# Performance work log

Hardware: AMD Instinct MI355X
Metric: run time of the kernel (lower is better)

## Reference

```python
import jax, jax.numpy as jnp
import numpy as np

NEG_SLOPE = 0.2


def _add_self_loops(src, dst, n_nodes):
    loop = jnp.arange(n_nodes, dtype=src.dtype)
    return jnp.concatenate([src, loop]), jnp.concatenate([dst, loop])


def _gat_conv(x, W, a_src, a_dst, b, src, dst, n_nodes):
    # Linear transform: [N, F_out]
    h = x @ W
    # Per-node attention halves (heads=1)
    alpha_src = h @ a_src  # [N]
    alpha_dst = h @ a_dst  # [N]
    # Per-edge logits (gather) + LeakyReLU
    e = jax.nn.leaky_relu(alpha_src[src] + alpha_dst[dst], NEG_SLOPE)  # [E]
    # Segment softmax over incoming edges of each destination node
    m = jax.ops.segment_max(e, dst, num_segments=n_nodes)
    e = jnp.exp(e - m[dst])
    s = jax.ops.segment_sum(e, dst, num_segments=n_nodes)
    alpha = e / (s[dst] + 1e-16)  # [E]
    # Weighted scatter-add aggregation
    out = jax.ops.segment_sum(h[src] * alpha[:, None], dst, num_segments=n_nodes)
    return out + b


def setup_inputs() -> dict:
    key = jax.random.key(0)
    ks = jax.random.split(key, 10)
    N, E, D_IN, D_HID, D_OUT = 100000, 3200000, 128, 128, 64
    x = jax.random.normal(ks[0], (N, D_IN), dtype=jnp.float32)
    edge_index = jax.random.randint(ks[1], (2, E), 0, N, dtype=jnp.int64)
    # Glorot-ish scaled params
    W1 = jax.random.normal(ks[2], (D_IN, D_HID), dtype=jnp.float32) / np.sqrt(D_IN)
    a1_src = jax.random.normal(ks[3], (D_HID,), dtype=jnp.float32) / np.sqrt(D_HID)
    a1_dst = jax.random.normal(ks[4], (D_HID,), dtype=jnp.float32) / np.sqrt(D_HID)
    b1 = jnp.zeros((D_HID,), dtype=jnp.float32)
    W2 = jax.random.normal(ks[5], (D_HID, D_OUT), dtype=jnp.float32) / np.sqrt(D_HID)
    a2_src = jax.random.normal(ks[6], (D_OUT,), dtype=jnp.float32) / np.sqrt(D_OUT)
    a2_dst = jax.random.normal(ks[7], (D_OUT,), dtype=jnp.float32) / np.sqrt(D_OUT)
    b2 = jnp.zeros((D_OUT,), dtype=jnp.float32)
    return {"x": x, "edge_index": edge_index, "W1": W1, "a1_src": a1_src,
            "a1_dst": a1_dst, "b1": b1, "W2": W2, "a2_src": a2_src,
            "a2_dst": a2_dst, "b2": b2}


def reference(x, edge_index, W1, a1_src, a1_dst, b1, W2, a2_src, a2_dst, b2):
    n_nodes = x.shape[0]
    # PyG GATConv default: add self-loops
    src, dst = _add_self_loops(edge_index[0], edge_index[1], n_nodes)
    h = jax.nn.relu(_gat_conv(x, W1, a1_src, a1_dst, b1, src, dst, n_nodes))
    h = _gat_conv(h, W2, a2_src, a2_dst, b2, src, dst, n_nodes)
    return jnp.mean(h, axis=0)  # [output_dim]
```

## Files before the change

### kernel.cpp

```cpp
#include <hip/hip_runtime.h>
#include <cstdint>
#include <cstddef>

#define LEAKY_SLOPE 0.2f

typedef __attribute__((ext_vector_type(8))) short short8;
typedef __attribute__((ext_vector_type(4))) float f32x4;

static __device__ inline unsigned short f2b(float f) {
  union { float f; unsigned int u; } c; c.f = f;
  unsigned int u = c.u;
  unsigned int r = (u + 0x7fffu + ((u >> 16) & 1u)) >> 16;
  return (unsigned short)r;
}
static __device__ inline float b2f(unsigned short b) {
  union { unsigned int u; float f; } c; c.u = ((unsigned int)b) << 16;
  return c.f;
}
static __device__ inline unsigned char f2f8(float v) {
  int pk = __builtin_amdgcn_cvt_pk_fp8_f32(v, v, 0, false);
  return (unsigned char)(pk & 0xff);
}
static __device__ inline void fma8f8(float* acc, uint2 u, float w) {
  auto a = __builtin_amdgcn_cvt_pk_f32_fp8(u.x, false);
  auto b = __builtin_amdgcn_cvt_pk_f32_fp8(u.x, true);
  auto c = __builtin_amdgcn_cvt_pk_f32_fp8(u.y, false);
  auto d = __builtin_amdgcn_cvt_pk_f32_fp8(u.y, true);
  acc[0] += w * a[0]; acc[1] += w * a[1];
  acc[2] += w * b[0]; acc[3] += w * b[1];
  acc[4] += w * c[0]; acc[5] += w * c[1];
  acc[6] += w * d[0]; acc[7] += w * d[1];
}

__global__ __launch_bounds__(256) void k_bhist(const int* __restrict__ dst,
                                               int* __restrict__ gcount,
                                               int E, int N, int NB) {
  __shared__ int lh[512];
  for (int i = threadIdx.x; i < NB; i += 256) lh[i] = 0;
  __syncthreads();
  int stride = gridDim.x * blockDim.x;
  for (int idx = blockIdx.x * blockDim.x + threadIdx.x; idx < E + N; idx += stride) {
    int d = (idx < E) ? dst[idx] : (idx - E);
    atomicAdd(&lh[d >> 8], 1);
  }
  __syncthreads();
  for (int i = threadIdx.x; i < NB; i += 256)
    if (lh[i]) atomicAdd(&gcount[i], lh[i]);
}

__global__ __launch_bounds__(512) void k_bscan(const int* __restrict__ gcount,
                                               int* __restrict__ gbase,
                                               int* __restrict__ gcursor,
                                               int NB, int ET, int* __restrict__ offN) {
  __shared__ int sm[512];
  int t = threadIdx.x;
  int v = (t < NB) ? gcount[t] : 0;
  sm[t] = v;
  __syncthreads();
  for (int o = 1; o < 512; o <<= 1) {
    int x = (t >= o) ? sm[t - o] : 0;
    __syncthreads();
    sm[t] += x;
    __syncthreads();
  }
  if (t < NB) {
    int b = sm[t] - v;
    gbase[t] = b;
    gcursor[t] = b;
  }
  if (t == 0) { gbase[NB] = ET; *offN = ET; }
}

template <int CHUNK>
__global__ __launch_bounds__(256) void k_binpass(const int* __restrict__ src,
                                                 const int* __restrict__ dst,
                                                 int* __restrict__ gcursor,
                                                 unsigned int* __restrict__ staging,
                                                 int E, int N, int NB) {
  __shared__ int lh[512];
  __shared__ int lbase[512];
  const int t = threadIdx.x;
  const int ET = E + N;
  const int e0 = blockIdx.x * CHUNK;
  const int e1 = min(e0 + CHUNK, ET);
  for (int i = t; i < NB; i += 256) lh[i] = 0;
  __syncthreads();
  for (int i = e0 + t; i < e1; i += 256) {
    int d = (i < E) ? dst[i] : (i - E);
    atomicAdd(&lh[d >> 8], 1);
  }
  __syncthreads();
  for (int i = t; i < NB; i += 256) {
    int c = lh[i];
    lbase[i] = c ? atomicAdd(&gcursor[i], c) : 0;
    lh[i] = 0;
  }
  __syncthreads();
  for (int i = e0 + t; i < e1; i += 256) {
    int s, d;
    if (i < E) { s = src[i]; d = dst[i]; }
    else       { s = d = i - E; }
    int b = d >> 8;
    int r = atomicAdd(&lh[b], 1);
    staging[lbase[b] + r] = ((unsigned int)s << 8) | (unsigned int)(d & 255);
  }
}

__global__ __launch_bounds__(256) void k_csrbuild(const int* __restrict__ gbase,
                                                  const unsigned int* __restrict__ staging,
                                                  int* __restrict__ off,
                                                  int* __restrict__ csr,
                                                  int N) {
  __shared__ int sc[256];
  __shared__ int cur[256];
  const int b = blockIdx.x, t = threadIdx.x;
  const int s0 = gbase[b], s1 = gbase[b + 1];
  cur[t] = 0;
  __syncthreads();
  for (int i = s0 + t; i < s1; i += 256)
    atomicAdd(&cur[staging[i] & 255], 1);
  __syncthreads();
  int v = cur[t];
  sc[t] = v;
  __syncthreads();
  for (int o = 1; o < 256; o <<= 1) {
    int x = (t >= o) ? sc[t - o] : 0;
    __syncthreads();
    sc[t] += x;
    __syncthreads();
  }
  int excl = s0 + sc[t] - v;
  int node = b * 256 + t;
  if (node < N) off[node] = excl;
  __syncthreads();
  cur[t] = excl;
  __syncthreads();
  for (int i = s0 + t; i < s1; i += 256) {
    unsigned int pv = staging[i];
    int slot = atomicAdd(&cur[pv & 255], 1);
    csr[slot] = (int)(pv >> 8);
  }
}

__global__ __launch_bounds__(256) void k_prep_w(const float* __restrict__ W1,
                                                const float* __restrict__ W2,
                                                unsigned short* __restrict__ W1t,
                                                unsigned short* __restrict__ W2t) {
  int t = threadIdx.x;
  for (int o = t; o < 128 * 128; o += 256) {
    int n = o >> 7, k = o & 127;
    W1t[o] = f2b(W1[k * 128 + n]);
  }
  for (int o = t; o < 64 * 128; o += 256) {
    int n = o >> 7, k = o & 127;
    W2t[o] = f2b(W2[k * 64 + n]);
  }
}

template <int COLS, bool SRC_F32>
__global__ __launch_bounds__(256) void k_gemm_bf16(const void* __restrict__ Ap,
                                                   const unsigned short* __restrict__ Bt,
                                                   unsigned char* __restrict__ C,
                                                   const float* __restrict__ av_src,
                                                   const float* __restrict__ av_dst,
                                                   float* __restrict__ as_,
                                                   float* __restrict__ ad_,
                                                   int N) {
  constexpr int K = 128;
  constexpr int LDA = K + 8;
  __shared__ __align__(16) unsigned short As[64 * LDA];
  __shared__ __align__(16) unsigned short Bs[COLS * LDA];
  const int t = threadIdx.x;
  const int wave = t >> 6, lane = t & 63;
  const int row0 = blockIdx.x * 64;

#pragma unroll
  for (int i = 0; i < 4; ++i) {
    int c = t + 256 * i;
    int r = c >> 4, cq = c & 15;
    int4 v = make_int4(0, 0, 0, 0);
    if (row0 + r < N) {
      if constexpr (SRC_F32) {
        const float* Ar = (const float*)Ap + (size_t)(row0 + r) * K + cq * 8;
        float4 u = *reinterpret_cast<const float4*>(Ar);
        float4 w = *reinterpret_cast<const float4*>(Ar + 4);
        v.x = (int)f2b(u.x) | ((int)f2b(u.y) << 16);
        v.y = (int)f2b(u.z) | ((int)f2b(u.w) << 16);
        v.z = (int)f2b(w.x) | ((int)f2b(w.y) << 16);
        v.w = (int)f2b(w.z) | ((int)f2b(w.w) << 16);
      } else {
        v = *reinterpret_cast<const int4*>((const unsigned short*)Ap +
                                           (size_t)(row0 + r) * K + cq * 8);
      }
    }
    *reinterpret_cast<int4*>(&As[r * LDA + cq * 8]) = v;
  }
#pragma unroll
  for (int i = 0; i < COLS / 16; ++i) {
    int c = t + 256 * i;
    int r = c >> 4, cq = c & 15;
    *reinterpret_cast<int4*>(&Bs[r * LDA + cq * 8]) =
        *reinterpret_cast<const int4*>(Bt + (size_t)r * K + cq * 8);
  }
  __syncthreads();

  const int m15 = lane & 15;
  const int koff = (lane >> 4) * 8;
  const int arow = wave * 16 + m15;

  f32x4 acc[COLS / 16];
#pragma unroll
  for (int ct = 0; ct < COLS / 16; ++ct) acc[ct] = (f32x4){0.f, 0.f, 0.f, 0.f};

#pragma unroll
  for (int kk = 0; kk < K / 32; ++kk) {
    short8 af = *reinterpret_cast<const short8*>(&As[arow * LDA + kk * 32 + koff]);
#pragma unroll
    for (int ct = 0; ct < COLS / 16; ++ct) {
      short8 bf = *reinterpret_cast<const short8*>(&Bs[(ct * 16 + m15) * LDA + kk * 32 + koff]);
      acc[ct] = __builtin_amdgcn_mfma_f32_16x16x32_bf16(af, bf, acc[ct], 0, 0, 0);
    }
  }

#pragma unroll
  for (int ct = 0; ct < COLS / 16; ++ct) {
#pragma unroll
    for (int r = 0; r < 4; ++r) {
      int grow = row0 + wave * 16 + (lane >> 4) * 4 + r;
      if (grow < N)
        C[(size_t)grow * COLS + ct * 16 + m15] = f2f8(acc[ct][r]);
    }
  }

  {
    float ps[4] = {0.f, 0.f, 0.f, 0.f}, pd[4] = {0.f, 0.f, 0.f, 0.f};
#pragma unroll
    for (int ct = 0; ct < COLS / 16; ++ct) {
      float av = av_src[ct * 16 + m15];
      float bv = av_dst[ct * 16 + m15];
#pragma unroll
      for (int r = 0; r < 4; ++r) {
        ps[r] += acc[ct][r] * av;
        pd[r] += acc[ct][r] * bv;
      }
    }
#pragma unroll
    for (int o = 1; o < 16; o <<= 1) {
#pragma unroll
      for (int r = 0; r < 4; ++r) {
        ps[r] += __shfl_xor(ps[r], o);
        pd[r] += __shfl_xor(pd[r], o);
      }
    }
    if (m15 == 0) {
#pragma unroll
      for (int r = 0; r < 4; ++r) {
        int grow = row0 + wave * 16 + (lane >> 4) * 4 + r;
        if (grow < N) { as_[grow] = ps[r]; ad_[grow] = pd[r]; }
      }
    }
  }
}

template <int F, int DEPTH, bool RELU, bool OUT_BF16>
__global__ __launch_bounds__(256) void k_agg(const int* __restrict__ off,
                                             const int* __restrict__ csr,
                                             const float* __restrict__ as_,
                                             const float* __restrict__ ad_,
                                             const unsigned char* __restrict__ h,
                                             const float* __restrict__ bias,
                                             void* __restrict__ outp, int N) {
  constexpr int LPR = F / 8;
  constexpr int GPI = 64 / LPR;
  int wid = (blockIdx.x * blockDim.x + threadIdx.x) >> 6;
  int lane = threadIdx.x & 63;
  if (wid >= N) return;
  const int s0 = off[wid], s1 = off[wid + 1];
  const float adv = ad_[wid];
  const int g  = lane / LPR;
  const int fl = lane % LPR;
  const unsigned char* hb = h + (size_t)fl * 8;

  float acc[8] = {0.f, 0.f, 0.f, 0.f, 0.f, 0.f, 0.f, 0.f};
  float lsum = 0.f;

  for (int base = s0; base < s1; base += 64) {
    int i = base + lane;
    int sv = 0;
    float wexp = 0.f;
    if (i < s1) {
      sv = csr[i];
      float e = as_[sv] + adv;
      e = (e > 0.f) ? e : LEAKY_SLOPE * e;
      wexp = __expf(e);
      lsum += wexp;
    }
    const int jn = min(64, s1 - base);
    int jj = 0;
    for (; jj + DEPTH * GPI <= jn; jj += DEPTH * GPI) {
      int sj[DEPTH];
      float wv[DEPTH];
      uint2 u[DEPTH];
#pragma unroll
      for (int k = 0; k < DEPTH; ++k) {
        sj[k] = __shfl(sv, jj + g + k * GPI);
        wv[k] = __shfl(wexp, jj + g + k * GPI);
      }
#pragma unroll
      for (int k = 0; k < DEPTH; ++k)
        u[k] = *reinterpret_cast<const uint2*>(hb + (size_t)sj[k] * F);
#pragma unroll
      for (int k = 0; k < DEPTH; ++k)
        fma8f8(acc, u[k], wv[k]);
    }
    for (; jj < jn; jj += GPI) {
      int sj0 = __shfl(sv, jj + g);
      float w0 = __shfl(wexp, jj + g);
      uint2 u0 = *reinterpret_cast<const uint2*>(hb + (size_t)sj0 * F);
      fma8f8(acc, u0, w0);
    }
  }

  for (int o = 32; o; o >>= 1) lsum += __shfl_xor(lsum, o);
  const float inv_s = 1.f / (lsum + 1e-16f);

#pragma unroll
  for (int o = LPR; o < 64; o <<= 1) {
#pragma unroll
    for (int k = 0; k < 8; ++k) acc[k] += __shfl_xor(acc[k], o);
  }

  if (g == 0) {
    float ov[8];
#pragma unroll
    for (int k = 0; k < 8; ++k) {
      ov[k] = acc[k] * inv_s + bias[fl * 8 + k];
      if (RELU) ov[k] = fmaxf(ov[k], 0.f);
    }
    if constexpr (OUT_BF16) {
      int4 pk;
      pk.x = (int)f2b(ov[0]) | ((int)f2b(ov[1]) << 16);
      pk.y = (int)f2b(ov[2]) | ((int)f2b(ov[3]) << 16);
      pk.z = (int)f2b(ov[4]) | ((int)f2b(ov[5]) << 16);
      pk.w = (int)f2b(ov[6]) | ((int)f2b(ov[7]) << 16);
      *reinterpret_cast<int4*>((unsigned short*)outp + (size_t)wid * F + fl * 8) = pk;
    } else {
      float* op = (float*)outp + (size_t)wid * F + fl * 8;
      *reinterpret_cast<float4*>(op) = make_float4(ov[0], ov[1], ov[2], ov[3]);
      *reinterpret_cast<float4*>(op + 4) = make_float4(ov[4], ov[5], ov[6], ov[7]);
    }
  }
}

__global__ __launch_bounds__(256) void k_mean(const float* __restrict__ out2,
                                              float* __restrict__ d_out, int N) {
  int c = threadIdx.x & 63;
  int w = threadIdx.x >> 6;
  float acc = 0.f;
  for (int r = blockIdx.x * 4 + w; r < N; r += gridDim.x * 4)
    acc += out2[(size_t)r * 64 + c];
  atomicAdd(&d_out[c], acc * (1.0f / (float)N));
}

extern "C" void kernel_launch(void* const* d_in, const int* in_sizes, int n_in,
                              void* d_out, int out_size, void* d_ws, size_t ws_size,
                              hipStream_t stream) {
  (void)n_in; (void)out_size; (void)ws_size;
  const float* x      = (const float*)d_in[0];
  const int*   edges  = (const int*)d_in[1];
  const float* W1     = (const float*)d_in[2];
  const float* a1_src = (const float*)d_in[3];
  const float* a1_dst = (const float*)d_in[4];
  const float* b1     = (const float*)d_in[5];
  const float* W2     = (const float*)d_in[6];
  const float* a2_src = (const float*)d_in[7];
  const float* a2_dst = (const float*)d_in[8];
  const float* b2     = (const float*)d_in[9];
  float* out = (float*)d_out;

  const int N = in_sizes[0] / 128;
  const int E = in_sizes[1] / 2;
  const int ET = E + N;
  const int NB = (N + 255) >> 8;

  const int* e_src = edges;
  const int* e_dst = edges + E;

  char* ws = (char*)d_ws;
  size_t o = 0;
  auto alloc = [&](size_t bytes) {
    size_t p = o;
    o += (bytes + 511) & ~(size_t)511;
    return p;
  };
  unsigned char*  h1f = (unsigned char*)(ws + alloc((size_t)N * 128));
  unsigned short* g1b = (unsigned short*)(ws + alloc((size_t)N * 128 * 2));
  unsigned char*  h2f = (unsigned char*)(ws + alloc((size_t)N * 64));
  float* out2   = (float*)(ws + alloc((size_t)N * 64 * 4));
  float* as1    = (float*)(ws + alloc((size_t)N * 4));
  float* ad1    = (float*)(ws + alloc((size_t)N * 4));
  float* as2    = (float*)(ws + alloc((size_t)N * 4));
  float* ad2    = (float*)(ws + alloc((size_t)N * 4));
  int*   off    = (int*)(ws + alloc((size_t)(N + 1) * 4));
  int*   gcount = (int*)(ws + alloc((size_t)(NB + 1) * 4));
  int*   gbase  = (int*)(ws + alloc((size_t)(NB + 1) * 4));
  int*   gcursor= (int*)(ws + alloc((size_t)(NB + 1) * 4));
  unsigned int* staging = (unsigned int*)(ws + alloc((size_t)ET * 4));
  int*   csr    = (int*)(ws + alloc((size_t)ET * 4));
  unsigned short* W1t = (unsigned short*)(ws + alloc((size_t)128 * 128 * 2));
  unsigned short* W2t = (unsigned short*)(ws + alloc((size_t)64 * 128 * 2));

  hipMemsetAsync(gcount, 0, (size_t)NB * 4, stream);
  k_bhist<<<512, 256, 0, stream>>>(e_dst, gcount, E, N, NB);
  k_bscan<<<1, 512, 0, stream>>>(gcount, gbase, gcursor, NB, ET, off + N);
  constexpr int CHUNK = 8192;
  k_binpass<CHUNK><<<(ET + CHUNK - 1) / CHUNK, 256, 0, stream>>>(
      e_src, e_dst, gcursor, staging, E, N, NB);
  k_csrbuild<<<NB, 256, 0, stream>>>(gbase, staging, off, csr, N);

  k_prep_w<<<1, 256, 0, stream>>>(W1, W2, W1t, W2t);

  const int gemm_grid = (N + 63) / 64;
  const int node_wave_grid = (N + 3) / 4;

  k_gemm_bf16<128, true><<<gemm_grid, 256, 0, stream>>>(
      x, W1t, h1f, a1_src, a1_dst, as1, ad1, N);
  k_agg<128, 8, true, true><<<node_wave_grid, 256, 0, stream>>>(
      off, csr, as1, ad1, h1f, b1, (void*)g1b, N);

  k_gemm_bf16<64, false><<<gemm_grid, 256, 0, stream>>>(
      g1b, W2t, h2f, a2_src, a2_dst, as2, ad2, N);
  k_agg<64, 4, false, false><<<node_wave_grid, 256, 0, stream>>>(
      off, csr, as2, ad2, h2f, b2, (void*)out2, N);

  hipMemsetAsync(out, 0, 64 * sizeof(float), stream);
  k_mean<<<256, 256, 0, stream>>>(out2, out, N);
}
```

Measured before the change: 445.3 us.

## Collapse second GAT layer into per-source coefficients using linearity of mean

The second layer's full aggregation and GEMM are replaced by an algebraic shortcut. Because the output is a mean over nodes, it equals W2 applied to a coefficient-weighted sum of layer-1 features plus b2, where each coefficient is the sum of the normalized attention weights on a source's out-edges. Layer-2 attention logits are computed in the layer-1 aggregation epilogue through the precomputed vectors W2·a2_src and W2·a2_dst, and a coefficient kernel scatters them with atomics. This removes the 64-wide edge gather and the N×64 intermediate, at the cost of scattered float atomics and small numeric differences in accumulation order. The layer-1 accumulation is also rewritten to use packed two-wide float FMAs.

```diff
diff --git a/kernel.cpp b/kernel.cpp
--- a/kernel.cpp
+++ b/kernel.cpp
@@ -6,6 +6,7 @@
 
 typedef __attribute__((ext_vector_type(8))) short short8;
 typedef __attribute__((ext_vector_type(4))) float f32x4;
+typedef __attribute__((ext_vector_type(2))) float f32x2;
 
 static __device__ inline unsigned short f2b(float f) {
   union { float f; unsigned int u; } c; c.f = f;
@@ -20,16 +21,6 @@
 static __device__ inline unsigned char f2f8(float v) {
   int pk = __builtin_amdgcn_cvt_pk_fp8_f32(v, v, 0, false);
   return (unsigned char)(pk & 0xff);
-}
-static __device__ inline void fma8f8(float* acc, uint2 u, float w) {
-  auto a = __builtin_amdgcn_cvt_pk_f32_fp8(u.x, false);
-  auto b = __builtin_amdgcn_cvt_pk_f32_fp8(u.x, true);
-  auto c = __builtin_amdgcn_cvt_pk_f32_fp8(u.y, false);
-  auto d = __builtin_amdgcn_cvt_pk_f32_fp8(u.y, true);
-  acc[0] += w * a[0]; acc[1] += w * a[1];
-  acc[2] += w * b[0]; acc[3] += w * b[1];
-  acc[4] += w * c[0]; acc[5] += w * c[1];
-  acc[6] += w * d[0]; acc[7] += w * d[1];
 }
 
 __global__ __launch_bounds__(256) void k_bhist(const int* __restrict__ dst,
@@ -144,29 +135,37 @@
 
 __global__ __launch_bounds__(256) void k_prep_w(const float* __restrict__ W1,
                                                 const float* __restrict__ W2,
+                                                const float* __restrict__ a2_src,
+                                                const float* __restrict__ a2_dst,
                                                 unsigned short* __restrict__ W1t,
-                                                unsigned short* __restrict__ W2t) {
+                                                float* __restrict__ va_s,
+                                                float* __restrict__ va_d) {
   int t = threadIdx.x;
   for (int o = t; o < 128 * 128; o += 256) {
     int n = o >> 7, k = o & 127;
     W1t[o] = f2b(W1[k * 128 + n]);
   }
-  for (int o = t; o < 64 * 128; o += 256) {
-    int n = o >> 7, k = o & 127;
-    W2t[o] = f2b(W2[k * 64 + n]);
-  }
-}
-
-template <int COLS, bool SRC_F32>
-__global__ __launch_bounds__(256) void k_gemm_bf16(const void* __restrict__ Ap,
-                                                   const unsigned short* __restrict__ Bt,
-                                                   unsigned char* __restrict__ C,
-                                                   const float* __restrict__ av_src,
-                                                   const float* __restrict__ av_dst,
-                                                   float* __restrict__ as_,
-                                                   float* __restrict__ ad_,
-                                                   int N) {
-  constexpr int K = 128;
+  if (t < 128) {
+    float s = 0.f, d = 0.f;
+    for (int c = 0; c < 64; ++c) {
+      float w = W2[t * 64 + c];
+      s += w * a2_src[c];
+      d += w * a2_dst[c];
+    }
+    va_s[t] = s;
+    va_d[t] = d;
+  }
+}
+
+__global__ __launch_bounds__(256) void k_gemm1(const float* __restrict__ Ap,
+                                               const unsigned short* __restrict__ Bt,
+                                               unsigned char* __restrict__ C,
+                                               const float* __restrict__ av_src,
+                                               const float* __restrict__ av_dst,
+                                               float* __restrict__ as_,
+                                               float* __restrict__ ad_,
+                                               int N) {
+  constexpr int K = 128, COLS = 128;
   constexpr int LDA = K + 8;
   __shared__ __align__(16) unsigned short As[64 * LDA];
   __shared__ __align__(16) unsigned short Bs[COLS * LDA];
@@ -180,18 +179,13 @@
     int r = c >> 4, cq = c & 15;
     int4 v = make_int4(0, 0, 0, 0);
     if (row0 + r < N) {
-      if constexpr (SRC_F32) {
-        const float* Ar = (const float*)Ap + (size_t)(row0 + r) * K + cq * 8;
-        float4 u = *reinterpret_cast<const float4*>(Ar);
-        float4 w = *reinterpret_cast<const float4*>(Ar + 4);
-        v.x = (int)f2b(u.x) | ((int)f2b(u.y) << 16);
-        v.y = (int)f2b(u.z) | ((int)f2b(u.w) << 16);
-        v.z = (int)f2b(w.x) | ((int)f2b(w.y) << 16);
-        v.w = (int)f2b(w.z) | ((int)f2b(w.w) << 16);
-      } else {
-        v = *reinterpret_cast<const int4*>((const unsigned short*)Ap +
-                                           (size_t)(row0 + r) * K + cq * 8);
-      }
+      const float* Ar = Ap + (size_t)(row0 + r) * K + cq * 8;
+      float4 u = *reinterpret_cast<const float4*>(Ar);
+      float4 w = *reinterpret_cast<const float4*>(Ar + 4);
+      v.x = (int)f2b(u.x) | ((int)f2b(u.y) << 16);
+      v.y = (int)f2b(u.z) | ((int)f2b(u.w) << 16);
+      v.z = (int)f2b(w.x) | ((int)f2b(w.y) << 16);
+      v.w = (int)f2b(w.z) | ((int)f2b(w.w) << 16);
     }
     *reinterpret_cast<int4*>(&As[r * LDA + cq * 8]) = v;
   }
@@ -262,16 +256,20 @@
   }
 }
 
-template <int F, int DEPTH, bool RELU, bool OUT_BF16>
-__global__ __launch_bounds__(256) void k_agg(const int* __restrict__ off,
-                                             const int* __restrict__ csr,
-                                             const float* __restrict__ as_,
-                                             const float* __restrict__ ad_,
-                                             const unsigned char* __restrict__ h,
-                                             const float* __restrict__ bias,
-                                             void* __restrict__ outp, int N) {
-  constexpr int LPR = F / 8;
-  constexpr int GPI = 64 / LPR;
+template <int DEPTH>
+__global__ __launch_bounds__(256) void k_agg1(const int* __restrict__ off,
+                                              const int* __restrict__ csr,
+                                              const float* __restrict__ as_,
+                                              const float* __restrict__ ad_,
+                                              const unsigned char* __restrict__ h,
+                                              const float* __restrict__ bias,
+                                              const float* __restrict__ va_s,
+                                              const float* __restrict__ va_d,
+                                              unsigned short* __restrict__ g1,
+                                              float* __restrict__ as2,
+                                              float* __restrict__ ad2,
+                                              int N) {
+  constexpr int F = 128, LPR = 16, GPI = 4;
   int wid = (blockIdx.x * blockDim.x + threadIdx.x) >> 6;
   int lane = threadIdx.x & 63;
   if (wid >= N) return;
@@ -281,7 +279,7 @@
   const int fl = lane % LPR;
   const unsigned char* hb = h + (size_t)fl * 8;
 
-  float acc[8] = {0.f, 0.f, 0.f, 0.f, 0.f, 0.f, 0.f, 0.f};
+  f32x2 acc2[4] = {{0.f, 0.f}, {0.f, 0.f}, {0.f, 0.f}, {0.f, 0.f}};
   float lsum = 0.f;
 
   for (int base = s0; base < s1; base += 64) {
@@ -310,14 +308,23 @@
       for (int k = 0; k < DEPTH; ++k)
         u[k] = *reinterpret_cast<const uint2*>(hb + (size_t)sj[k] * F);
 #pragma unroll
-      for (int k = 0; k < DEPTH; ++k)
-        fma8f8(acc, u[k], wv[k]);
+      for (int k = 0; k < DEPTH; ++k) {
+        f32x2 w2 = {wv[k], wv[k]};
+        acc2[0] += w2 * __builtin_amdgcn_cvt_pk_f32_fp8(u[k].x, false);
+        acc2[1] += w2 * __builtin_amdgcn_cvt_pk_f32_fp8(u[k].x, true);
+        acc2[2] += w2 * __builtin_amdgcn_cvt_pk_f32_fp8(u[k].y, false);
+        acc2[3] += w2 * __builtin_amdgcn_cvt_pk_f32_fp8(u[k].y, true);
+      }
     }
     for (; jj < jn; jj += GPI) {
       int sj0 = __shfl(sv, jj + g);
       float w0 = __shfl(wexp, jj + g);
       uint2 u0 = *reinterpret_cast<const uint2*>(hb + (size_t)sj0 * F);
-      fma8f8(acc, u0, w0);
+      f32x2 w2 = {w0, w0};
+      acc2[0] += w2 * __builtin_amdgcn_cvt_pk_f32_fp8(u0.x, false);
+      acc2[1] += w2 * __builtin_amdgcn_cvt_pk_f32_fp8(u0.x, true);
+      acc2[2] += w2 * __builtin_amdgcn_cvt_pk_f32_fp8(u0.y, false);
+      acc2[3] += w2 * __builtin_amdgcn_cvt_pk_f32_fp8(u0.y, true);
     }
   }
 
@@ -327,39 +334,95 @@
 #pragma unroll
   for (int o = LPR; o < 64; o <<= 1) {
 #pragma unroll
-    for (int k = 0; k < 8; ++k) acc[k] += __shfl_xor(acc[k], o);
+    for (int k = 0; k < 4; ++k) {
+      acc2[k][0] += __shfl_xor(acc2[k][0], o);
+      acc2[k][1] += __shfl_xor(acc2[k][1], o);
+    }
   }
 
   if (g == 0) {
     float ov[8];
 #pragma unroll
     for (int k = 0; k < 8; ++k) {
-      ov[k] = acc[k] * inv_s + bias[fl * 8 + k];
-      if (RELU) ov[k] = fmaxf(ov[k], 0.f);
-    }
-    if constexpr (OUT_BF16) {
-      int4 pk;
-      pk.x = (int)f2b(ov[0]) | ((int)f2b(ov[1]) << 16);
-      pk.y = (int)f2b(ov[2]) | ((int)f2b(ov[3]) << 16);
-      pk.z = (int)f2b(ov[4]) | ((int)f2b(ov[5]) << 16);
-      pk.w = (int)f2b(ov[6]) | ((int)f2b(ov[7]) << 16);
-      *reinterpret_cast<int4*>((unsigned short*)outp + (size_t)wid * F + fl * 8) = pk;
-    } else {
-      float* op = (float*)outp + (size_t)wid * F + fl * 8;
-      *reinterpret_cast<float4*>(op) = make_float4(ov[0], ov[1], ov[2], ov[3]);
-      *reinterpret_cast<float4*>(op + 4) = make_float4(ov[4], ov[5], ov[6], ov[7]);
-    }
-  }
-}
-
-__global__ __launch_bounds__(256) void k_mean(const float* __restrict__ out2,
-                                              float* __restrict__ d_out, int N) {
-  int c = threadIdx.x & 63;
-  int w = threadIdx.x >> 6;
+      ov[k] = fmaxf(acc2[k >> 1][k & 1] * inv_s + bias[fl * 8 + k], 0.f);
+    }
+    int4 pk;
+    pk.x = (int)f2b(ov[0]) | ((int)f2b(ov[1]) << 16);
+    pk.y = (int)f2b(ov[2]) | ((int)f2b(ov[3]) << 16);
+    pk.z = (int)f2b(ov[4]) | ((int)f2b(ov[5]) << 16);
+    pk.w = (int)f2b(ov[6]) | ((int)f2b(ov[7]) << 16);
+    *reinterpret_cast<int4*>(g1 + (size_t)wid * F + fl * 8) = pk;
+
+    float ps = 0.f, pd = 0.f;
+#pragma unroll
+    for (int k = 0; k < 8; ++k) {
+      ps += ov[k] * va_s[fl * 8 + k];
+      pd += ov[k] * va_d[fl * 8 + k];
+    }
+#pragma unroll
+    for (int o = 1; o < 16; o <<= 1) {
+      ps += __shfl_xor(ps, o);
+      pd += __shfl_xor(pd, o);
+    }
+    if (lane == 0) { as2[wid] = ps; ad2[wid] = pd; }
+  }
+}
+
+__global__ __launch_bounds__(256) void k_coef(const int* __restrict__ off,
+                                              const int* __restrict__ csr,
+                                              const float* __restrict__ as2,
+                                              const float* __restrict__ ad2,
+                                              float* __restrict__ C, int N) {
+  int wid = (blockIdx.x * blockDim.x + threadIdx.x) >> 6;
+  int lane = threadIdx.x & 63;
+  if (wid >= N) return;
+  const int s0 = off[wid], s1 = off[wid + 1];
+  const float adv = ad2[wid];
+
+  float lsum = 0.f;
+  for (int base = s0; base < s1; base += 64) {
+    int i = base + lane;
+    if (i < s1) {
+      float e = as2[csr[i]] + adv;
+      e = (e > 0.f) ? e : LEAKY_SLOPE * e;
+      lsum += __expf(e);
+    }
+  }
+  for (int o = 32; o; o >>= 1) lsum += __shfl_xor(lsum, o);
+  const float inv_s = 1.f / (lsum + 1e-16f);
+
+  for (int base = s0; base < s1; base += 64) {
+    int i = base + lane;
+    if (i < s1) {
+      int sv = csr[i];
+      float e = as2[sv] + adv;
+      e = (e > 0.f) ? e : LEAKY_SLOPE * e;
+      atomicAdd(&C[sv], __expf(e) * inv_s);
+    }
+  }
+}
+
+__global__ __launch_bounds__(256) void k_wsum(const unsigned short* __restrict__ g1,
+                                              const float* __restrict__ C,
+                                              float* __restrict__ v, int N) {
+  __shared__ float sm[256];
+  const int f = threadIdx.x & 127, half = threadIdx.x >> 7;
   float acc = 0.f;
-  for (int r = blockIdx.x * 4 + w; r < N; r += gridDim.x * 4)
-    acc += out2[(size_t)r * 64 + c];
-  atomicAdd(&d_out[c], acc * (1.0f / (float)N));
+  for (int r = blockIdx.x * 2 + half; r < N; r += gridDim.x * 2)
+    acc += C[r] * b2f(g1[(size_t)r * 128 + f]);
+  sm[threadIdx.x] = acc;
+  __syncthreads();
+  if (half == 0) atomicAdd(&v[f], sm[threadIdx.x] + sm[threadIdx.x + 128]);
+}
+
+__global__ __launch_bounds__(64) void k_finish(const float* __restrict__ v,
+                                               const float* __restrict__ W2,
+                                               const float* __restrict__ b2,
+                                               float* __restrict__ out, float invN) {
+  int c = threadIdx.x;
+  float s = 0.f;
+  for (int k = 0; k < 128; ++k) s += v[k] * W2[k * 64 + c];
+  out[c] = s * invN + b2[c];
 }
 
 extern "C" void kernel_launch(void* const* d_in, const int* in_sizes, int n_in,
@@ -395,12 +458,12 @@
   };
   unsigned char*  h1f = (unsigned char*)(ws + alloc((size_t)N * 128));
   unsigned short* g1b = (unsigned short*)(ws + alloc((size_t)N * 128 * 2));
-  unsigned char*  h2f = (unsigned char*)(ws + alloc((size_t)N * 64));
-  float* out2   = (float*)(ws + alloc((size_t)N * 64 * 4));
   float* as1    = (float*)(ws + alloc((size_t)N * 4));
   float* ad1    = (float*)(ws + alloc((size_t)N * 4));
   float* as2    = (float*)(ws + alloc((size_t)N * 4));
   float* ad2    = (float*)(ws + alloc((size_t)N * 4));
+  float* Cv     = (float*)(ws + alloc((size_t)N * 4));
+  float* vsum   = (float*)(ws + alloc(128 * 4));
   int*   off    = (int*)(ws + alloc((size_t)(N + 1) * 4));
   int*   gcount = (int*)(ws + alloc((size_t)(NB + 1) * 4));
   int*   gbase  = (int*)(ws + alloc((size_t)(NB + 1) * 4));
@@ -408,7 +471,8 @@
   unsigned int* staging = (unsigned int*)(ws + alloc((size_t)ET * 4));
   int*   csr    = (int*)(ws + alloc((size_t)ET * 4));
   unsigned short* W1t = (unsigned short*)(ws + alloc((size_t)128 * 128 * 2));
-  unsigned short* W2t = (unsigned short*)(ws + alloc((size_t)64 * 128 * 2));
+  float* va_s   = (float*)(ws + alloc(128 * 4));
+  float* va_d   = (float*)(ws + alloc(128 * 4));
 
   hipMemsetAsync(gcount, 0, (size_t)NB * 4, stream);
   k_bhist<<<512, 256, 0, stream>>>(e_dst, gcount, E, N, NB);
@@ -418,21 +482,18 @@
       e_src, e_dst, gcursor, staging, E, N, NB);
   k_csrbuild<<<NB, 256, 0, stream>>>(gbase, staging, off, csr, N);
 
-  k_prep_w<<<1, 256, 0, stream>>>(W1, W2, W1t, W2t);
+  k_prep_w<<<1, 256, 0, stream>>>(W1, W2, a2_src, a2_dst, W1t, va_s, va_d);
+  hipMemsetAsync(Cv, 0, (size_t)N * 4, stream);
+  hipMemsetAsync(vsum, 0, 128 * 4, stream);
 
   const int gemm_grid = (N + 63) / 64;
   const int node_wave_grid = (N + 3) / 4;
 
-  k_gemm_bf16<128, true><<<gemm_grid, 256, 0, stream>>>(
-      x, W1t, h1f, a1_src, a1_dst, as1, ad1, N);
-  k_agg<128, 8, true, true><<<node_wave_grid, 256, 0, stream>>>(
-      off, csr, as1, ad1, h1f, b1, (void*)g1b, N);
-
-  k_gemm_bf16<64, false><<<gemm_grid, 256, 0, stream>>>(
-      g1b, W2t, h2f, a2_src, a2_dst, as2, ad2, N);
-  k_agg<64, 4, false, false><<<node_wave_grid, 256, 0, stream>>>(
-      off, csr, as2, ad2, h2f, b2, (void*)out2, N);
-
-  hipMemsetAsync(out, 0, 64 * sizeof(float), stream);
-  k_mean<<<256, 256, 0, stream>>>(out2, out, N);
-}
+  k_gemm1<<<gemm_grid, 256, 0, stream>>>(x, W1t, h1f, a1_src, a1_dst, as1, ad1, N);
+  k_agg1<8><<<node_wave_grid, 256, 0, stream>>>(
+      off, csr, as1, ad1, h1f, b1, va_s, va_d, g1b, as2, ad2, N);
+
+  k_coef<<<node_wave_grid, 256, 0, stream>>>(off, csr, as2, ad2, Cv, N);
+  k_wsum<<<512, 256, 0, stream>>>(g1b, Cv, vsum, N);
+  k_finish<<<1, 64, 0, stream>>>(vsum, W2, b2, out, 1.0f / (float)N);
+}
```

Result: slower. 523.8 us (+17.6%).

## Fuse layer-2 aggregation with mean reduction and use packed f32x2 FMAs

Applied to the files above, without the earlier changes.

The second aggregation kernel now runs as a persistent grid-stride kernel that accumulates each node's normalized output directly into per-wave mean accumulators. These are reduced through shared memory and atomically added into a 64-float buffer. This removes the N×64 fp32 out2 write and read and the separate k_mean kernel, and the bias is added once at the end. Both aggregation kernels also switch accumulation to f32x2 vectors so the compiler can emit packed FMA instructions. The cost is a fixed 1024-block grid for layer 2, which may balance load differently, plus an extra tiny finish kernel and memset.

```diff
diff --git a/kernel.cpp b/kernel.cpp
--- a/kernel.cpp
+++ b/kernel.cpp
@@ -6,6 +6,7 @@
 
 typedef __attribute__((ext_vector_type(8))) short short8;
 typedef __attribute__((ext_vector_type(4))) float f32x4;
+typedef __attribute__((ext_vector_type(2))) float f32x2;
 
 static __device__ inline unsigned short f2b(float f) {
   union { float f; unsigned int u; } c; c.f = f;
@@ -20,16 +21,6 @@
 static __device__ inline unsigned char f2f8(float v) {
   int pk = __builtin_amdgcn_cvt_pk_fp8_f32(v, v, 0, false);
   return (unsigned char)(pk & 0xff);
-}
-static __device__ inline void fma8f8(float* acc, uint2 u, float w) {
-  auto a = __builtin_amdgcn_cvt_pk_f32_fp8(u.x, false);
-  auto b = __builtin_amdgcn_cvt_pk_f32_fp8(u.x, true);
-  auto c = __builtin_amdgcn_cvt_pk_f32_fp8(u.y, false);
-  auto d = __builtin_amdgcn_cvt_pk_f32_fp8(u.y, true);
-  acc[0] += w * a[0]; acc[1] += w * a[1];
-  acc[2] += w * b[0]; acc[3] += w * b[1];
-  acc[4] += w * c[0]; acc[5] += w * c[1];
-  acc[6] += w * d[0]; acc[7] += w * d[1];
 }
 
 __global__ __launch_bounds__(256) void k_bhist(const int* __restrict__ dst,
@@ -262,16 +253,16 @@
   }
 }
 
-template <int F, int DEPTH, bool RELU, bool OUT_BF16>
-__global__ __launch_bounds__(256) void k_agg(const int* __restrict__ off,
-                                             const int* __restrict__ csr,
-                                             const float* __restrict__ as_,
-                                             const float* __restrict__ ad_,
-                                             const unsigned char* __restrict__ h,
-                                             const float* __restrict__ bias,
-                                             void* __restrict__ outp, int N) {
-  constexpr int LPR = F / 8;
-  constexpr int GPI = 64 / LPR;
+template <int DEPTH>
+__global__ __launch_bounds__(256) void k_agg1(const int* __restrict__ off,
+                                              const int* __restrict__ csr,
+                                              const float* __restrict__ as_,
+                                              const float* __restrict__ ad_,
+                                              const unsigned char* __restrict__ h,
+                                              const float* __restrict__ bias,
+                                              unsigned short* __restrict__ g1,
+                                              int N) {
+  constexpr int F = 128, LPR = 16, GPI = 4;
   int wid = (blockIdx.x * blockDim.x + threadIdx.x) >> 6;
   int lane = threadIdx.x & 63;
   if (wid >= N) return;
@@ -281,7 +272,7 @@
   const int fl = lane % LPR;
   const unsigned char* hb = h + (size_t)fl * 8;
 
-  float acc[8] = {0.f, 0.f, 0.f, 0.f, 0.f, 0.f, 0.f, 0.f};
+  f32x2 acc2[4] = {{0.f, 0.f}, {0.f, 0.f}, {0.f, 0.f}, {0.f, 0.f}};
   float lsum = 0.f;
 
   for (int base = s0; base < s1; base += 64) {
@@ -310,14 +301,23 @@
       for (int k = 0; k < DEPTH; ++k)
         u[k] = *reinterpret_cast<const uint2*>(hb + (size_t)sj[k] * F);
 #pragma unroll
-      for (int k = 0; k < DEPTH; ++k)
-        fma8f8(acc, u[k], wv[k]);
+      for (int k = 0; k < DEPTH; ++k) {
+        f32x2 w2 = {wv[k], wv[k]};
+        acc2[0] += w2 * __builtin_amdgcn_cvt_pk_f32_fp8(u[k].x, false);
+        acc2[1] += w2 * __builtin_amdgcn_cvt_pk_f32_fp8(u[k].x, true);
+        acc2[2] += w2 * __builtin_amdgcn_cvt_pk_f32_fp8(u[k].y, false);
+        acc2[3] += w2 * __builtin_amdgcn_cvt_pk_f32_fp8(u[k].y, true);
+      }
     }
     for (; jj < jn; jj += GPI) {
       int sj0 = __shfl(sv, jj + g);
       float w0 = __shfl(wexp, jj + g);
       uint2 u0 = *reinterpret_cast<const uint2*>(hb + (size_t)sj0 * F);
-      fma8f8(acc, u0, w0);
+      f32x2 w2 = {w0, w0};
+      acc2[0] += w2 * __builtin_amdgcn_cvt_pk_f32_fp8(u0.x, false);
+      acc2[1] += w2 * __builtin_amdgcn_cvt_pk_f32_fp8(u0.x, true);
+      acc2[2] += w2 * __builtin_amdgcn_cvt_pk_f32_fp8(u0.y, false);
+      acc2[3] += w2 * __builtin_amdgcn_cvt_pk_f32_fp8(u0.y, true);
     }
   }
 
@@ -327,39 +327,133 @@
 #pragma unroll
   for (int o = LPR; o < 64; o <<= 1) {
 #pragma unroll
-    for (int k = 0; k < 8; ++k) acc[k] += __shfl_xor(acc[k], o);
+    for (int k = 0; k < 4; ++k) {
+      acc2[k][0] += __shfl_xor(acc2[k][0], o);
+      acc2[k][1] += __shfl_xor(acc2[k][1], o);
+    }
   }
 
   if (g == 0) {
     float ov[8];
 #pragma unroll
-    for (int k = 0; k < 8; ++k) {
-      ov[k] = acc[k] * inv_s + bias[fl * 8 + k];
-      if (RELU) ov[k] = fmaxf(ov[k], 0.f);
-    }
-    if constexpr (OUT_BF16) {
-      int4 pk;
-      pk.x = (int)f2b(ov[0]) | ((int)f2b(ov[1]) << 16);
-      pk.y = (int)f2b(ov[2]) | ((int)f2b(ov[3]) << 16);
-      pk.z = (int)f2b(ov[4]) | ((int)f2b(ov[5]) << 16);
-      pk.w = (int)f2b(ov[6]) | ((int)f2b(ov[7]) << 16);
-      *reinterpret_cast<int4*>((unsigned short*)outp + (size_t)wid * F + fl * 8) = pk;
-    } else {
-      float* op = (float*)outp + (size_t)wid * F + fl * 8;
-      *reinterpret_cast<float4*>(op) = make_float4(ov[0], ov[1], ov[2], ov[3]);
-      *reinterpret_cast<float4*>(op + 4) = make_float4(ov[4], ov[5], ov[6], ov[7]);
-    }
-  }
-}
-
-__global__ __launch_bounds__(256) void k_mean(const float* __restrict__ out2,
-                                              float* __restrict__ d_out, int N) {
-  int c = threadIdx.x & 63;
-  int w = threadIdx.x >> 6;
-  float acc = 0.f;
-  for (int r = blockIdx.x * 4 + w; r < N; r += gridDim.x * 4)
-    acc += out2[(size_t)r * 64 + c];
-  atomicAdd(&d_out[c], acc * (1.0f / (float)N));
+    for (int k = 0; k < 8; ++k)
+      ov[k] = fmaxf(acc2[k >> 1][k & 1] * inv_s + bias[fl * 8 + k], 0.f);
+    int4 pk;
+    pk.x = (int)f2b(ov[0]) | ((int)f2b(ov[1]) << 16);
+    pk.y = (int)f2b(ov[2]) | ((int)f2b(ov[3]) << 16);
+    pk.z = (int)f2b(ov[4]) | ((int)f2b(ov[5]) << 16);
+    pk.w = (int)f2b(ov[6]) | ((int)f2b(ov[7]) << 16);
+    *reinterpret_cast<int4*>(g1 + (size_t)wid * F + fl * 8) = pk;
+  }
+}
+
+template <int DEPTH>
+__global__ __launch_bounds__(256) void k_agg2m(const int* __restrict__ off,
+                                               const int* __restrict__ csr,
+                                               const float* __restrict__ as_,
+                                               const float* __restrict__ ad_,
+                                               const unsigned char* __restrict__ h,
+                                               float* __restrict__ vsum,
+                                               int N, float invN) {
+  constexpr int F = 64, LPR = 8, GPI = 8;
+  const int lane = threadIdx.x & 63;
+  const int wv = (blockIdx.x * blockDim.x + threadIdx.x) >> 6;
+  const int nw = (gridDim.x * blockDim.x) >> 6;
+  const int g  = lane >> 3;
+  const int fl = lane & 7;
+  const unsigned char* hb = h + (size_t)fl * 8;
+
+  f32x2 macc[4] = {{0.f, 0.f}, {0.f, 0.f}, {0.f, 0.f}, {0.f, 0.f}};
+
+  for (int wid = wv; wid < N; wid += nw) {
+    const int s0 = off[wid], s1 = off[wid + 1];
+    const float adv = ad_[wid];
+    f32x2 acc2[4] = {{0.f, 0.f}, {0.f, 0.f}, {0.f, 0.f}, {0.f, 0.f}};
+    float lsum = 0.f;
+
+    for (int base = s0; base < s1; base += 64) {
+      int i = base + lane;
+      int sv = 0;
+      float wexp = 0.f;
+      if (i < s1) {
+        sv = csr[i];
+        float e = as_[sv] + adv;
+        e = (e > 0.f) ? e : LEAKY_SLOPE * e;
+        wexp = __expf(e);
+        lsum += wexp;
+      }
+      const int jn = min(64, s1 - base);
+      int jj = 0;
+      for (; jj + DEPTH * GPI <= jn; jj += DEPTH * GPI) {
+        int sj[DEPTH];
+        float wvv[DEPTH];
+        uint2 u[DEPTH];
+#pragma unroll
+        for (int k = 0; k < DEPTH; ++k) {
+          sj[k] = __shfl(sv, jj + g + k * GPI);
+          wvv[k] = __shfl(wexp, jj + g + k * GPI);
+        }
+#pragma unroll
+        for (int k = 0; k < DEPTH; ++k)
+          u[k] = *reinterpret_cast<const uint2*>(hb + (size_t)sj[k] * F);
+#pragma unroll
+        for (int k = 0; k < DEPTH; ++k) {
+          f32x2 w2 = {wvv[k], wvv[k]};
+          acc2[0] += w2 * __builtin_amdgcn_cvt_pk_f32_fp8(u[k].x, false);
+          acc2[1] += w2 * __builtin_amdgcn_cvt_pk_f32_fp8(u[k].x, true);
+          acc2[2] += w2 * __builtin_amdgcn_cvt_pk_f32_fp8(u[k].y, false);
+          acc2[3] += w2 * __builtin_amdgcn_cvt_pk_f32_fp8(u[k].y, true);
+        }
+      }
+      for (; jj < jn; jj += GPI) {
+        int sj0 = __shfl(sv, jj + g);
+        float w0 = __shfl(wexp, jj + g);
+        uint2 u0 = *reinterpret_cast<const uint2*>(hb + (size_t)sj0 * F);
+        f32x2 w2 = {w0, w0};
+        acc2[0] += w2 * __builtin_amdgcn_cvt_pk_f32_fp8(u0.x, false);
+        acc2[1] += w2 * __builtin_amdgcn_cvt_pk_f32_fp8(u0.x, true);
+        acc2[2] += w2 * __builtin_amdgcn_cvt_pk_f32_fp8(u0.y, false);
+        acc2[3] += w2 * __builtin_amdgcn_cvt_pk_f32_fp8(u0.y, true);
+      }
+    }
+
+    for (int o = 32; o; o >>= 1) lsum += __shfl_xor(lsum, o);
+    f32x2 inv_s = {1.f / (lsum + 1e-16f), 1.f / (lsum + 1e-16f)};
+#pragma unroll
+    for (int k = 0; k < 4; ++k) macc[k] += inv_s * acc2[k];
+  }
+
+#pragma unroll
+  for (int o = LPR; o < 64; o <<= 1) {
+#pragma unroll
+    for (int k = 0; k < 4; ++k) {
+      macc[k][0] += __shfl_xor(macc[k][0], o);
+      macc[k][1] += __shfl_xor(macc[k][1], o);
+    }
+  }
+
+  __shared__ float sm[4 * 64];
+  const int wloc = threadIdx.x >> 6;
+  if (g == 0) {
+#pragma unroll
+    for (int k = 0; k < 4; ++k) {
+      sm[wloc * 64 + fl * 8 + 2 * k]     = macc[k][0];
+      sm[wloc * 64 + fl * 8 + 2 * k + 1] = macc[k][1];
+    }
+  }
+  __syncthreads();
+  if (threadIdx.x < 64) {
+    float s = sm[threadIdx.x] + sm[64 + threadIdx.x] +
+              sm[128 + threadIdx.x] + sm[192 + threadIdx.x];
+    atomicAdd(&vsum[threadIdx.x], s * invN);
+  }
+}
+
+__global__ __launch_bounds__(64) void k_finish(const float* __restrict__ v,
+                                               const float* __restrict__ b2,
+                                               float* __restrict__ out) {
+  int c = threadIdx.x;
+  out[c] = v[c] + b2[c];
 }
 
 extern "C" void kernel_launch(void* const* d_in, const int* in_sizes, int n_in,
@@ -396,11 +490,11 @@
   unsigned char*  h1f = (unsigned char*)(ws + alloc((size_t)N * 128));
   unsigned short* g1b = (unsigned short*)(ws + alloc((size_t)N * 128 * 2));
   unsigned char*  h2f = (unsigned char*)(ws + alloc((size_t)N * 64));
-  float* out2   = (float*)(ws + alloc((size_t)N * 64 * 4));
   float* as1    = (float*)(ws + alloc((size_t)N * 4));
   float* ad1    = (float*)(ws + alloc((size_t)N * 4));
   float* as2    = (float*)(ws + alloc((size_t)N * 4));
   float* ad2    = (float*)(ws + alloc((size_t)N * 4));
+  float* vsum   = (float*)(ws + alloc(64 * 4));
   int*   off    = (int*)(ws + alloc((size_t)(N + 1) * 4));
   int*   gcount = (int*)(ws + alloc((size_t)(NB + 1) * 4));
   int*   gbase  = (int*)(ws + alloc((size_t)(NB + 1) * 4));
@@ -419,20 +513,19 @@
   k_csrbuild<<<NB, 256, 0, stream>>>(gbase, staging, off, csr, N);
 
   k_prep_w<<<1, 256, 0, stream>>>(W1, W2, W1t, W2t);
+  hipMemsetAsync(vsum, 0, 64 * 4, stream);
 
   const int gemm_grid = (N + 63) / 64;
   const int node_wave_grid = (N + 3) / 4;
 
   k_gemm_bf16<128, true><<<gemm_grid, 256, 0, stream>>>(
       x, W1t, h1f, a1_src, a1_dst, as1, ad1, N);
-  k_agg<128, 8, true, true><<<node_wave_grid, 256, 0, stream>>>(
-      off, csr, as1, ad1, h1f, b1, (void*)g1b, N);
+  k_agg1<8><<<node_wave_grid, 256, 0, stream>>>(
+      off, csr, as1, ad1, h1f, b1, g1b, N);
 
   k_gemm_bf16<64, false><<<gemm_grid, 256, 0, stream>>>(
       g1b, W2t, h2f, a2_src, a2_dst, as2, ad2, N);
-  k_agg<64, 4, false, false><<<node_wave_grid, 256, 0, stream>>>(
-      off, csr, as2, ad2, h2f, b2, (void*)out2, N);
-
-  hipMemsetAsync(out, 0, 64 * sizeof(float), stream);
-  k_mean<<<256, 256, 0, stream>>>(out2, out, N);
-}
+  k_agg2m<4><<<1024, 256, 0, stream>>>(off, csr, as2, ad2, h2f, vsum, N,
+                                       1.0f / (float)N);
+  k_finish<<<1, 64, 0, stream>>>(vsum, b2, out);
+}
```

After: 391.5 us. 12.1% less time.
